# Optimization experiments

Measured on AMD Instinct MI355X. Metric: run time of the kernel, lower is better.

The kernel has to match this reference:

```python
import jax, jax.numpy as jnp
import numpy as np

S, B, H = 4096, 128, 128
D_WIN = 2.0
SIGMA = D_WIN / 2.0


def setup_inputs() -> dict:
    key = jax.random.key(0)
    k1, k2, k3, k4, k5, k6 = jax.random.split(key, 6)
    return {
        "e": jax.random.normal(k1, (S, B, H), dtype=jnp.float32),
        "d": jax.random.normal(k2, (1, B, H), dtype=jnp.float32),
        "W_a": jax.random.normal(k3, (H, H), dtype=jnp.float32),
        "W_p": jax.random.normal(k4, (H, H), dtype=jnp.float32),
        "v_p": jax.random.normal(k5, (H, 1), dtype=jnp.float32),
        "W_c": jax.random.normal(k6, (2 * H, H), dtype=jnp.float32),
    }


def reference(e, d, W_a, W_p, v_p, W_c):
    s = e.shape[0]
    # alignment: scores over source positions, softmax along S (dim 0)
    scores = jnp.einsum('sbh,sbh->sb', e, jnp.broadcast_to(d @ W_a, e.shape))  # [S,B]
    a = jax.nn.softmax(scores, axis=0)
    # predictive position p_t in [0, S]
    p_t = (s * jax.nn.sigmoid(jnp.tanh(d @ W_p) @ v_p)).squeeze()  # [B]
    pos = jnp.arange(s, dtype=e.dtype)[:, None]                    # [S,1]
    diff = p_t[None, :] - pos                                      # [S,B]
    mask = (jnp.abs(diff) <= D_WIN).astype(e.dtype)
    gauss = jnp.exp(-(diff ** 2) / (2.0 * SIGMA ** 2)) * mask
    w = a * gauss                                                  # [S,B]
    context = jnp.einsum('sbh,sb->bh', e, w)[None]                 # [1,B,H]
    x = jnp.concatenate([context, d], axis=2)                      # [1,B,2H]
    output = jnp.tanh(x @ W_c)                                     # [1,B,H]
    return output, w
```

## Files before the change

### kernel.cpp

```cpp
#include <hip/hip_runtime.h>
#include <math.h>

#define S_DIM 4096
#define B_DIM 128
#define H_DIM 128
#define NBLK  32
#define CHUNK (S_DIM / NBLK)
#define NEG_BIG -1e30f

__global__ __launch_bounds__(128) void k_prep(
    const float* __restrict__ d, const float* __restrict__ Wa,
    const float* __restrict__ Wp, const float* __restrict__ vp,
    float* __restrict__ dWa, float* __restrict__ pt)
{
    int b = blockIdx.x;
    int h = threadIdx.x;
    __shared__ float db[H_DIM];
    db[h] = d[b * H_DIM + h];
    __syncthreads();
    float aa = 0.f, ap = 0.f;
    #pragma unroll 4
    for (int k = 0; k < H_DIM; ++k) {
        float dk = db[k];
        aa = fmaf(dk, Wa[k * H_DIM + h], aa);
        ap = fmaf(dk, Wp[k * H_DIM + h], ap);
    }
    dWa[b * H_DIM + h] = aa;
    float r = tanhf(ap) * vp[h];
    #pragma unroll
    for (int o = 1; o < 64; o <<= 1) r += __shfl_xor(r, o);
    __shared__ float red[2];
    if ((h & 63) == 0) red[h >> 6] = r;
    __syncthreads();
    if (h == 0) {
        float sum = red[0] + red[1];
        pt[b] = (float)S_DIM / (1.f + __expf(-sum));
    }
}

__global__ __launch_bounds__(256) void k_scores(
    const float* __restrict__ e, const float* __restrict__ dWa,
    const float* __restrict__ pt,
    float* __restrict__ pm, float* __restrict__ pl, float* __restrict__ win)
{
    int b    = blockIdx.x;
    int blk  = blockIdx.y;
    int tid  = threadIdx.x;
    int wave = tid >> 6;
    int lane = tid & 63;
    int half = lane >> 5;
    int hl   = lane & 31;

    float4 wf = ((const float4*)(dWa + b * H_DIM))[hl];
    float ptb = pt[b];
    int   s0  = (int)floorf(ptb) - 2;

    int sbase = blk * CHUNK + wave * 2 + half;
    const float* ep = e + (size_t)sbase * (B_DIM * H_DIM) + b * H_DIM + hl * 4;
    const size_t stride = (size_t)8 * B_DIM * H_DIM;

    float mloc = NEG_BIG, lloc = 0.f;
    float4 ev = *(const float4*)ep;
    #pragma unroll 4
    for (int i = 0; i < CHUNK / 8; ++i) {
        float4 cur = ev;
        if (i < CHUNK / 8 - 1) ev = *(const float4*)(ep + (size_t)(i + 1) * stride);
        float v = cur.x * wf.x + cur.y * wf.y + cur.z * wf.z + cur.w * wf.w;
        v += __shfl_xor(v, 1);
        v += __shfl_xor(v, 2);
        v += __shfl_xor(v, 4);
        v += __shfl_xor(v, 8);
        v += __shfl_xor(v, 16);
        if (v > mloc) { lloc = lloc * __expf(mloc - v) + 1.f; mloc = v; }
        else          { lloc += __expf(v - mloc); }
        if (hl == 0) {
            int s = sbase + i * 8;
            int idx = s - s0;
            if (idx >= 0 && idx < 5) {
                float diff = ptb - (float)s;
                if (fabsf(diff) <= 2.0f) win[b * 5 + idx] = v;
            }
        }
    }
    __shared__ float ms[8], ls[8];
    if (hl == 0) { ms[wave * 2 + half] = mloc; ls[wave * 2 + half] = lloc; }
    __syncthreads();
    if (tid == 0) {
        float M = NEG_BIG;
        #pragma unroll
        for (int j = 0; j < 8; ++j) M = fmaxf(M, ms[j]);
        float L = 0.f;
        #pragma unroll
        for (int j = 0; j < 8; ++j) L += ls[j] * __expf(ms[j] - M);
        pm[b * NBLK + blk] = M;
        pl[b * NBLK + blk] = L;
    }
}

__global__ __launch_bounds__(128) void k_final(
    const float* __restrict__ e, const float* __restrict__ d,
    const float* __restrict__ Wc,
    const float* __restrict__ pm, const float* __restrict__ pl,
    const float* __restrict__ win, const float* __restrict__ pt,
    float* __restrict__ out)
{
    int b = blockIdx.x;
    int t = threadIdx.x;

    __shared__ float sh[2];
    __shared__ float wv[5];
    __shared__ float x[2 * H_DIM];

    if (t < 64) {
        float m = (t < NBLK) ? pm[b * NBLK + t] : NEG_BIG;
        float l = (t < NBLK) ? pl[b * NBLK + t] : 0.f;
        float M = m;
        #pragma unroll
        for (int o = 1; o < 64; o <<= 1) M = fmaxf(M, __shfl_xor(M, o));
        float ls = l * __expf(m - M);
        #pragma unroll
        for (int o = 1; o < 64; o <<= 1) ls += __shfl_xor(ls, o);
        if (t == 0) { sh[0] = M; sh[1] = ls; }
    }
    __syncthreads();
    float M = sh[0], L = sh[1];
    float ptb = pt[b];
    int   s0  = (int)floorf(ptb) - 2;

    if (t < 5) {
        int s = s0 + t;
        float v = 0.f;
        if (s >= 0 && s < S_DIM) {
            float diff = ptb - (float)s;
            if (fabsf(diff) <= 2.0f) {
                v = __expf(win[b * 5 + t] - M) / L * __expf(-0.5f * diff * diff);
                out[B_DIM * H_DIM + (size_t)s * B_DIM + b] = v;
            }
        }
        wv[t] = v;
    }
    __syncthreads();

    float ctx = 0.f;
    #pragma unroll
    for (int k = 0; k < 5; ++k) {
        int s = s0 + k;
        if (s >= 0 && s < S_DIM)
            ctx = fmaf(wv[k], e[(size_t)s * (B_DIM * H_DIM) + b * H_DIM + t], ctx);
    }
    x[t] = ctx;
    x[H_DIM + t] = d[b * H_DIM + t];
    __syncthreads();

    float acc = 0.f;
    #pragma unroll 4
    for (int j = 0; j < 2 * H_DIM; ++j)
        acc = fmaf(x[j], Wc[j * H_DIM + t], acc);
    out[b * H_DIM + t] = tanhf(acc);
}

extern "C" void kernel_launch(void* const* d_in, const int* in_sizes, int n_in,
                              void* d_out, int out_size, void* d_ws, size_t ws_size,
                              hipStream_t stream)
{
    const float* e  = (const float*)d_in[0];
    const float* d  = (const float*)d_in[1];
    const float* Wa = (const float*)d_in[2];
    const float* Wp = (const float*)d_in[3];
    const float* vp = (const float*)d_in[4];
    const float* Wc = (const float*)d_in[5];
    float* out = (float*)d_out;

    float* ws  = (float*)d_ws;
    float* dWa = ws;
    float* pt  = ws + 16384;
    float* pm  = ws + 16512;
    float* pl  = ws + 20608;
    float* win = ws + 24704;

    hipMemsetAsync(out + B_DIM * H_DIM, 0, (size_t)S_DIM * B_DIM * sizeof(float), stream);

    k_prep  <<<B_DIM, H_DIM, 0, stream>>>(d, Wa, Wp, vp, dWa, pt);
    k_scores<<<dim3(B_DIM, NBLK), 256, 0, stream>>>(e, dWa, pt, pm, pl, win);
    k_final <<<B_DIM, H_DIM, 0, stream>>>(e, d, Wc, pm, pl, win, pt, out);
}
```

Baseline: 413.9 us.

## Batch all e loads up front in score kernel; split-K prep and final matvecs

The score kernel now issues all 16 float4 loads per thread before any compute. The shuffle reductions are interleaved across the 16 values, and the online softmax is replaced by a single max-then-sum pass. This exposes memory-level parallelism on the dominant 256MB stream of e. The prep and final kernels move to 256 threads and split the K dimension in half, with partial sums combined through shared memory. This shortens their serial matvec loops but raises register pressure in the score kernel. The prep kernel also keeps a __syncthreads inside a branch that only threads below 128 take, which is divergent and risky.

```diff
diff --git a/kernel.cpp b/kernel.cpp
--- a/kernel.cpp
+++ b/kernel.cpp
@@ -8,33 +8,43 @@
 #define CHUNK (S_DIM / NBLK)
 #define NEG_BIG -1e30f
 
-__global__ __launch_bounds__(128) void k_prep(
+__global__ __launch_bounds__(256) void k_prep(
     const float* __restrict__ d, const float* __restrict__ Wa,
     const float* __restrict__ Wp, const float* __restrict__ vp,
     float* __restrict__ dWa, float* __restrict__ pt)
 {
-    int b = blockIdx.x;
-    int h = threadIdx.x;
+    int b  = blockIdx.x;
+    int t  = threadIdx.x;
+    int h  = t & 127;
+    int kh = t >> 7;
     __shared__ float db[H_DIM];
-    db[h] = d[b * H_DIM + h];
+    if (t < H_DIM) db[t] = d[b * H_DIM + t];
     __syncthreads();
     float aa = 0.f, ap = 0.f;
-    #pragma unroll 4
-    for (int k = 0; k < H_DIM; ++k) {
+    int k0 = kh * 64;
+    #pragma unroll 8
+    for (int k = k0; k < k0 + 64; ++k) {
         float dk = db[k];
         aa = fmaf(dk, Wa[k * H_DIM + h], aa);
         ap = fmaf(dk, Wp[k * H_DIM + h], ap);
     }
-    dWa[b * H_DIM + h] = aa;
-    float r = tanhf(ap) * vp[h];
-    #pragma unroll
-    for (int o = 1; o < 64; o <<= 1) r += __shfl_xor(r, o);
-    __shared__ float red[2];
-    if ((h & 63) == 0) red[h >> 6] = r;
-    __syncthreads();
-    if (h == 0) {
-        float sum = red[0] + red[1];
-        pt[b] = (float)S_DIM / (1.f + __expf(-sum));
+    __shared__ float paa[256], pap[256];
+    paa[t] = aa; pap[t] = ap;
+    __syncthreads();
+    if (t < H_DIM) {
+        float a2 = paa[t] + paa[t + 128];
+        float p2 = pap[t] + pap[t + 128];
+        dWa[b * H_DIM + t] = a2;
+        float r = tanhf(p2) * vp[t];
+        #pragma unroll
+        for (int o = 1; o < 64; o <<= 1) r += __shfl_xor(r, o);
+        __shared__ float red[2];
+        if ((t & 63) == 0) red[t >> 6] = r;
+        __syncthreads();
+        if (t == 0) {
+            float sum = red[0] + red[1];
+            pt[b] = (float)S_DIM / (1.f + __expf(-sum));
+        }
     }
 }
 
@@ -50,54 +60,68 @@
     int lane = tid & 63;
     int half = lane >> 5;
     int hl   = lane & 31;
+    int halfIdx = wave * 2 + half;
 
     float4 wf = ((const float4*)(dWa + b * H_DIM))[hl];
     float ptb = pt[b];
     int   s0  = (int)floorf(ptb) - 2;
 
-    int sbase = blk * CHUNK + wave * 2 + half;
+    int sbase = blk * CHUNK + halfIdx;
     const float* ep = e + (size_t)sbase * (B_DIM * H_DIM) + b * H_DIM + hl * 4;
-    const size_t stride = (size_t)8 * B_DIM * H_DIM;
-
-    float mloc = NEG_BIG, lloc = 0.f;
-    float4 ev = *(const float4*)ep;
-    #pragma unroll 4
-    for (int i = 0; i < CHUNK / 8; ++i) {
-        float4 cur = ev;
-        if (i < CHUNK / 8 - 1) ev = *(const float4*)(ep + (size_t)(i + 1) * stride);
-        float v = cur.x * wf.x + cur.y * wf.y + cur.z * wf.z + cur.w * wf.w;
-        v += __shfl_xor(v, 1);
-        v += __shfl_xor(v, 2);
-        v += __shfl_xor(v, 4);
-        v += __shfl_xor(v, 8);
-        v += __shfl_xor(v, 16);
-        if (v > mloc) { lloc = lloc * __expf(mloc - v) + 1.f; mloc = v; }
-        else          { lloc += __expf(v - mloc); }
-        if (hl == 0) {
-            int s = sbase + i * 8;
+    const size_t stride8 = (size_t)8 * B_DIM * H_DIM;
+
+    float4 ev[16];
+    #pragma unroll
+    for (int j = 0; j < 16; ++j)
+        ev[j] = *(const float4*)(ep + (size_t)j * stride8);
+
+    float v[16];
+    #pragma unroll
+    for (int j = 0; j < 16; ++j)
+        v[j] = ev[j].x * wf.x + ev[j].y * wf.y + ev[j].z * wf.z + ev[j].w * wf.w;
+
+    #pragma unroll
+    for (int o = 1; o < 32; o <<= 1) {
+        #pragma unroll
+        for (int j = 0; j < 16; ++j)
+            v[j] += __shfl_xor(v[j], o);
+    }
+
+    float M = v[0];
+    #pragma unroll
+    for (int j = 1; j < 16; ++j) M = fmaxf(M, v[j]);
+    float L = 0.f;
+    #pragma unroll
+    for (int j = 0; j < 16; ++j) L += __expf(v[j] - M);
+
+    if (hl == 0) {
+        #pragma unroll
+        for (int j = 0; j < 16; ++j) {
+            int s = sbase + 8 * j;
             int idx = s - s0;
             if (idx >= 0 && idx < 5) {
                 float diff = ptb - (float)s;
-                if (fabsf(diff) <= 2.0f) win[b * 5 + idx] = v;
+                if (fabsf(diff) <= 2.0f) win[b * 5 + idx] = v[j];
             }
         }
     }
+
     __shared__ float ms[8], ls[8];
-    if (hl == 0) { ms[wave * 2 + half] = mloc; ls[wave * 2 + half] = lloc; }
+    if (hl == 0) { ms[halfIdx] = M; ls[halfIdx] = L; }
     __syncthreads();
     if (tid == 0) {
-        float M = NEG_BIG;
-        #pragma unroll
-        for (int j = 0; j < 8; ++j) M = fmaxf(M, ms[j]);
-        float L = 0.f;
-        #pragma unroll
-        for (int j = 0; j < 8; ++j) L += ls[j] * __expf(ms[j] - M);
-        pm[b * NBLK + blk] = M;
-        pl[b * NBLK + blk] = L;
-    }
-}
-
-__global__ __launch_bounds__(128) void k_final(
+        float Mb = NEG_BIG;
+        #pragma unroll
+        for (int j = 0; j < 8; ++j) Mb = fmaxf(Mb, ms[j]);
+        float Lb = 0.f;
+        #pragma unroll
+        for (int j = 0; j < 8; ++j) Lb += ls[j] * __expf(ms[j] - Mb);
+        pm[b * NBLK + blk] = Mb;
+        pl[b * NBLK + blk] = Lb;
+    }
+}
+
+__global__ __launch_bounds__(256) void k_final(
     const float* __restrict__ e, const float* __restrict__ d,
     const float* __restrict__ Wc,
     const float* __restrict__ pm, const float* __restrict__ pl,
@@ -110,6 +134,7 @@
     __shared__ float sh[2];
     __shared__ float wv[5];
     __shared__ float x[2 * H_DIM];
+    __shared__ float part[2][H_DIM];
 
     if (t < 64) {
         float m = (t < NBLK) ? pm[b * NBLK + t] : NEG_BIG;
@@ -141,22 +166,31 @@
     }
     __syncthreads();
 
-    float ctx = 0.f;
-    #pragma unroll
-    for (int k = 0; k < 5; ++k) {
-        int s = s0 + k;
-        if (s >= 0 && s < S_DIM)
-            ctx = fmaf(wv[k], e[(size_t)s * (B_DIM * H_DIM) + b * H_DIM + t], ctx);
-    }
-    x[t] = ctx;
-    x[H_DIM + t] = d[b * H_DIM + t];
-    __syncthreads();
-
+    if (t < H_DIM) {
+        float ctx = 0.f;
+        #pragma unroll
+        for (int k = 0; k < 5; ++k) {
+            int s = s0 + k;
+            if (s >= 0 && s < S_DIM)
+                ctx = fmaf(wv[k], e[(size_t)s * (B_DIM * H_DIM) + b * H_DIM + t], ctx);
+        }
+        x[t] = ctx;
+    } else {
+        x[t] = d[b * H_DIM + (t - H_DIM)];
+    }
+    __syncthreads();
+
+    int h  = t & 127;
+    int jh = t >> 7;
     float acc = 0.f;
-    #pragma unroll 4
-    for (int j = 0; j < 2 * H_DIM; ++j)
-        acc = fmaf(x[j], Wc[j * H_DIM + t], acc);
-    out[b * H_DIM + t] = tanhf(acc);
+    int j0 = jh * H_DIM;
+    #pragma unroll 8
+    for (int j = j0; j < j0 + H_DIM; ++j)
+        acc = fmaf(x[j], Wc[j * H_DIM + h], acc);
+    part[jh][h] = acc;
+    __syncthreads();
+    if (t < H_DIM)
+        out[b * H_DIM + t] = tanhf(part[0][t] + part[1][t]);
 }
 
 extern "C" void kernel_launch(void* const* d_in, const int* in_sizes, int n_in,
@@ -180,7 +214,7 @@
 
     hipMemsetAsync(out + B_DIM * H_DIM, 0, (size_t)S_DIM * B_DIM * sizeof(float), stream);
 
-    k_prep  <<<B_DIM, H_DIM, 0, stream>>>(d, Wa, Wp, vp, dWa, pt);
+    k_prep  <<<B_DIM, 256, 0, stream>>>(d, Wa, Wp, vp, dWa, pt);
     k_scores<<<dim3(B_DIM, NBLK), 256, 0, stream>>>(e, dWa, pt, pm, pl, win);
-    k_final <<<B_DIM, H_DIM, 0, stream>>>(e, d, Wc, pm, pl, win, pt, out);
-}
+    k_final <<<B_DIM, 256, 0, stream>>>(e, d, Wc, pm, pl, win, pt, out);
+}
```

New measurement: 381.3 us. 1.09x faster.
